# Performance work log

Hardware: AMD Instinct MI355X
Metric: run time of the kernel (lower is better)

Reference implementation:

```python
import jax, jax.numpy as jnp
import numpy as np

B, T = 1, 2048
N_EMBD = 4096
N_HEAD = 32
N_GROUPS = 8
HEAD = 128
Q_PER_KV = N_HEAD // N_GROUPS  # 4
WINDOW = 1024
EPS = 1e-5
ROPE_THETA = 10000.0


def setup_inputs() -> dict:
    key = jax.random.key(0)
    k0, k1, k2 = jax.random.split(key, 3)
    x = jax.random.normal(k0, (B, T, N_EMBD), dtype=jnp.float32)
    # RoPE tables: cos/sin of shape [T, HEAD] (rotary_percentage=1.0)
    inv_freq = 1.0 / (ROPE_THETA ** (jnp.arange(0, HEAD, 2, dtype=jnp.float32) / HEAD))
    ang = jnp.arange(T, dtype=jnp.float32)[:, None] * inv_freq[None, :]  # [T, HEAD//2]
    ang = jnp.concatenate([ang, ang], axis=-1)  # [T, HEAD]
    cos, sin = jnp.cos(ang), jnp.sin(ang)
    qkv_out = (N_HEAD + 2 * N_GROUPS) * HEAD  # 6144
    W_qkv = jax.random.normal(k1, (qkv_out, N_EMBD), dtype=jnp.float32) * 0.02
    W_proj = jax.random.normal(k2, (N_EMBD, N_HEAD * HEAD), dtype=jnp.float32) * 0.02
    norm_q_w = jnp.ones((N_HEAD * HEAD,), dtype=jnp.float32)
    norm_k_w = jnp.ones((N_GROUPS * HEAD,), dtype=jnp.float32)
    return {"x": x, "cos": cos, "sin": sin, "W_qkv": W_qkv,
            "norm_q_w": norm_q_w, "norm_k_w": norm_k_w, "W_proj": W_proj}


def _rmsnorm(x, w):
    # RMSNorm over last dim, matching litgpt RMSNorm (eps inside sqrt)
    var = jnp.mean(x * x, axis=-1, keepdims=True)
    return x * jax.lax.rsqrt(var + EPS) * w


def _apply_rope(x, cos, sin):
    # x: [B, H, T, D]; cos/sin: [T, D] (broadcast over B, H)
    d = x.shape[-1]
    x1, x2 = x[..., : d // 2], x[..., d // 2:]
    rotated = jnp.concatenate([-x2, x1], axis=-1)
    return x * cos + rotated * sin


def reference(x, cos, sin, W_qkv, norm_q_w, norm_k_w, W_proj):
    Bx, Tx, _ = x.shape
    qkv = jnp.einsum('btc,oc->bto', x, W_qkv)  # [B, T, (H+2G)*D]
    q_size = N_HEAD * HEAD
    kv_size = N_GROUPS * HEAD
    q = qkv[..., :q_size]
    k = qkv[..., q_size:q_size + kv_size]
    v = qkv[..., q_size + kv_size:]
    # norm_qk: RMSNorm over the full flattened q / k dims (pre head reshape)
    q = _rmsnorm(q, norm_q_w)
    k = _rmsnorm(k, norm_k_w)
    q = q.reshape(Bx, Tx, N_HEAD, HEAD).transpose(0, 2, 1, 3)     # [B, H, T, D]
    k = k.reshape(Bx, Tx, N_GROUPS, HEAD).transpose(0, 2, 1, 3)   # [B, G, T, D]
    v = v.reshape(Bx, Tx, N_GROUPS, HEAD).transpose(0, 2, 1, 3)   # [B, G, T, D]
    # rope_n_elem == head_size (rotary_percentage = 1.0)
    q = _apply_rope(q, cos, sin)
    k = _apply_rope(k, cos, sin)
    # GQA: expand kv groups to heads (repeat_interleave on head dim)
    k = jnp.repeat(k, Q_PER_KV, axis=1)  # [B, H, T, D]
    v = jnp.repeat(v, Q_PER_KV, axis=1)
    scale = 1.0 / jnp.sqrt(jnp.float32(HEAD))  # attention_scores_scalar is None
    scores = jnp.einsum('bhqd,bhkd->bhqk', q, k) * scale
    # causal + sliding-window mask: allowed iff 0 <= q_idx - kv_idx < WINDOW
    d = jnp.arange(Tx)[:, None] - jnp.arange(Tx)[None, :]
    bias = jnp.where((d >= 0) & (d < WINDOW), 0.0, -jnp.inf).astype(scores.dtype)
    attn = jax.nn.softmax(scores + bias, axis=-1)
    y = jnp.einsum('bhqk,bhkd->bhqd', attn, v)        # [B, H, T, D]
    y = y.transpose(0, 2, 1, 3).reshape(Bx, Tx, N_HEAD * HEAD)
    return jnp.einsum('bth,oh->bto', y, W_proj)       # [B, T, n_embd]
```

## Files before the change

### kernel.cpp

```cpp
#include <hip/hip_runtime.h>
#include <stdint.h>
#include <stddef.h>

#define T_SEQ 2048
#define WINDOW_SZ 1024

typedef __attribute__((ext_vector_type(4))) float f32x4;
typedef __attribute__((ext_vector_type(8))) short s16x8;

__device__ inline unsigned short f2bf(float f) {
  union { float f; unsigned u; } v; v.f = f;
  unsigned u = v.u;
  return (unsigned short)((u + 0x7fffu + ((u >> 16) & 1u)) >> 16);
}

__device__ inline void gld_lds16(const unsigned short* g, unsigned short* l) {
  __builtin_amdgcn_global_load_lds((const __attribute__((address_space(1))) void*)g,
                                   (__attribute__((address_space(3))) void*)l, 16, 0, 0);
}

__global__ __launch_bounds__(256) void cvt_bf16(const float* __restrict__ s,
                                                unsigned short* __restrict__ d, int n4) {
  int i = blockIdx.x * 256 + threadIdx.x;
  if (i >= n4) return;
  float4 v = ((const float4*)s)[i];
  ushort4 o;
  o.x = f2bf(v.x); o.y = f2bf(v.y); o.z = f2bf(v.z); o.w = f2bf(v.w);
  ((ushort4*)d)[i] = o;
}

__global__ __launch_bounds__(256) void gemm_bt(const unsigned short* __restrict__ A,
                                               const unsigned short* __restrict__ Bt,
                                               float* __restrict__ C, int M, int N, int K) {
  __shared__ unsigned short As[4096];
  __shared__ unsigned short Bs[4096];
  const int tid  = threadIdx.x;
  const int wave = tid >> 6, lane = tid & 63;
  const int quad = lane >> 4, l16 = lane & 15;
  const int m0 = blockIdx.y << 7, n0 = blockIdx.x << 7;
  const int wr = (wave >> 1) << 6;
  const int wc = (wave & 1) << 6;
  const int srow = tid >> 2;
  const int scol = (tid & 3) << 3;

  f32x4 acc[4][4] = {};

  const unsigned short* pA0 = A  + (size_t)(m0 + srow) * K + scol;
  const unsigned short* pA1 = A  + (size_t)(m0 + 64 + srow) * K + scol;
  const unsigned short* pB0 = Bt + (size_t)(n0 + srow) * K + scol;
  const unsigned short* pB1 = Bt + (size_t)(n0 + 64 + srow) * K + scol;
  unsigned short* lA0 = As + wave * 512;
  unsigned short* lA1 = As + 2048 + wave * 512;
  unsigned short* lB0 = Bs + wave * 512;
  unsigned short* lB1 = Bs + 2048 + wave * 512;

  for (int k0 = 0; k0 < K; k0 += 32) {
    gld_lds16(pA0 + k0, lA0);
    gld_lds16(pA1 + k0, lA1);
    gld_lds16(pB0 + k0, lB0);
    gld_lds16(pB1 + k0, lB1);
    __syncthreads();
    s16x8 af[4], bfr[4];
#pragma unroll
    for (int i = 0; i < 4; i++) {
      af[i]  = *(const s16x8*)&As[(wr + i * 16 + l16) * 32 + quad * 8];
      bfr[i] = *(const s16x8*)&Bs[(wc + i * 16 + l16) * 32 + quad * 8];
    }
#pragma unroll
    for (int mi = 0; mi < 4; mi++)
#pragma unroll
      for (int ni = 0; ni < 4; ni++)
        acc[mi][ni] = __builtin_amdgcn_mfma_f32_16x16x32_bf16(af[mi], bfr[ni], acc[mi][ni], 0, 0, 0);
    __syncthreads();
  }
#pragma unroll
  for (int mi = 0; mi < 4; mi++)
#pragma unroll
    for (int ni = 0; ni < 4; ni++) {
      int row = m0 + wr + mi * 16 + quad * 4;
      int col = n0 + wc + ni * 16 + l16;
#pragma unroll
      for (int r = 0; r < 4; r++)
        C[(size_t)(row + r) * N + col] = acc[mi][ni][r];
    }
}

__global__ __launch_bounds__(256) void normrope(const float* __restrict__ qkv,
                                                const float* __restrict__ cosb,
                                                const float* __restrict__ sinb,
                                                const float* __restrict__ wq,
                                                const float* __restrict__ wk,
                                                unsigned short* __restrict__ qr,
                                                unsigned short* __restrict__ kr,
                                                unsigned short* __restrict__ vt) {
  const int t = blockIdx.x, tid = threadIdx.x;
  const float* row = qkv + (size_t)t * 6144;
  float sq = 0.f, sk = 0.f;
#pragma unroll
  for (int i = 0; i < 4; i++) {
    float4 v = ((const float4*)row)[tid + i * 256];
    sq += v.x * v.x + v.y * v.y + v.z * v.z + v.w * v.w;
  }
  {
    float4 v = ((const float4*)(row + 4096))[tid];
    sk = v.x * v.x + v.y * v.y + v.z * v.z + v.w * v.w;
  }
#pragma unroll
  for (int off = 32; off; off >>= 1) { sq += __shfl_xor(sq, off); sk += __shfl_xor(sk, off); }
  __shared__ float red[8];
  if ((tid & 63) == 0) { red[tid >> 6] = sq; red[4 + (tid >> 6)] = sk; }
  __syncthreads();
  sq = red[0] + red[1] + red[2] + red[3];
  sk = red[4] + red[5] + red[6] + red[7];
  const float rq = rsqrtf(sq * (1.f / 4096.f) + 1e-5f) * (0.08838834764831845f * 1.4426950408889634f);
  const float rk = rsqrtf(sk * (1.f / 1024.f) + 1e-5f);
  for (int i = tid; i < 4096; i += 256) {
    int h = i >> 7, d = i & 127;
    int pd = (d < 64) ? d + 64 : d - 64;
    float val = row[i] * rq * wq[i];
    float pv  = row[(h << 7) + pd] * rq * wq[(h << 7) + pd];
    float rot = (d < 64) ? -pv : pv;
    float o = val * cosb[t * 128 + d] + rot * sinb[t * 128 + d];
    qr[(size_t)h * T_SEQ * 128 + t * 128 + d] = f2bf(o);
  }
  for (int i = tid; i < 1024; i += 256) {
    int g = i >> 7, d = i & 127;
    int pd = (d < 64) ? d + 64 : d - 64;
    float val = row[4096 + i] * rk * wk[i];
    float pv  = row[4096 + (g << 7) + pd] * rk * wk[(g << 7) + pd];
    float rot = (d < 64) ? -pv : pv;
    float o = val * cosb[t * 128 + d] + rot * sinb[t * 128 + d];
    kr[(size_t)g * T_SEQ * 128 + t * 128 + d] = f2bf(o);
  }
  for (int i = tid; i < 1024; i += 256) {
    int g = i >> 7, d = i & 127;
    vt[(size_t)g * 128 * T_SEQ + (size_t)d * T_SEQ + t] = f2bf(row[5120 + i]);
  }
}

__global__ __launch_bounds__(512, 2) void attn(const unsigned short* __restrict__ Q,
                                               const unsigned short* __restrict__ Kb,
                                               const unsigned short* __restrict__ Vt,
                                               unsigned short* __restrict__ Y) {
  __shared__ unsigned short Kbuf[2][64 * 128];
  __shared__ unsigned short Vbuf[2][128 * 64];
  __shared__ unsigned short Pbuf[8][2][16 * 72];
  const int qb = blockIdx.x, g = blockIdx.y;
  const int tid = threadIdx.x, wave = tid >> 6, lane = tid & 63;
  const int quad = lane >> 4, l16 = lane & 15;
  const int h = g * 4 + (wave >> 1);
  const int qbase = qb * 64;
  const int q0 = qbase + (wave & 1) * 32;
  const unsigned short* Qh = Q + (size_t)h * T_SEQ * 128;
  const unsigned short* Kg = Kb + (size_t)g * T_SEQ * 128;
  const unsigned short* Vg = Vt + (size_t)g * 128 * T_SEQ;

  s16x8 aq[2][4];
#pragma unroll
  for (int qt = 0; qt < 2; qt++)
#pragma unroll
    for (int ks = 0; ks < 4; ks++)
      aq[qt][ks] = *(const s16x8*)&Qh[(size_t)(q0 + qt * 16 + l16) * 128 + ks * 32 + quad * 8];

  f32x4 acc[2][8] = {};
  float lrow[2][4] = {};

  int lo = qbase - (WINDOW_SZ - 1);
  if (lo < 0) lo = 0;
  lo &= ~63;

#define STAGE_CHUNK(buf, kkv)                                                        \
  {                                                                                  \
    int kk_ = (kkv);                                                                 \
    _Pragma("unroll")                                                                \
    for (int j = 0; j < 2; j++) {                                                    \
      int rloc = wave * 8 + j * 4 + (lane >> 4);                                     \
      int oct = (lane & 15) ^ (rloc & 15);                                           \
      gld_lds16(Kg + (size_t)(kk_ + rloc) * 128 + oct * 8,                           \
                &Kbuf[buf][(wave * 8 + j * 4) * 128]);                               \
    }                                                                                \
    _Pragma("unroll")                                                                \
    for (int j = 0; j < 2; j++) {                                                    \
      int dloc = wave * 16 + j * 8 + (lane >> 3);                                    \
      int oct = (lane & 7) ^ (dloc & 7);                                             \
      gld_lds16(Vg + (size_t)dloc * T_SEQ + kk_ + oct * 8,                           \
                &Vbuf[buf][(wave * 16 + j * 8) * 64]);                               \
    }                                                                                \
  }

  STAGE_CHUNK(0, lo);
  int ib = 0;
  for (int kk = lo; kk < qbase + 64; kk += 64, ib ^= 1) {
    __syncthreads();
    if (kk + 64 < qbase + 64) STAGE_CHUNK(ib ^ 1, kk + 64);
    if (kk > q0 + 31 || kk + 63 < q0 - (WINDOW_SZ - 1)) continue;
    const unsigned short* kb = Kbuf[ib];
    const unsigned short* vb = Vbuf[ib];
    f32x4 sc[2][4] = {};
#pragma unroll
    for (int ks = 0; ks < 4; ks++) {
#pragma unroll
      for (int ci = 0; ci < 4; ci++) {
        s16x8 bk = *(const s16x8*)&kb[(ci * 16 + l16) * 128 + (((ks * 4 + quad) ^ l16) * 8)];
        sc[0][ci] = __builtin_amdgcn_mfma_f32_16x16x32_bf16(aq[0][ks], bk, sc[0][ci], 0, 0, 0);
        sc[1][ci] = __builtin_amdgcn_mfma_f32_16x16x32_bf16(aq[1][ks], bk, sc[1][ci], 0, 0, 0);
      }
    }
#pragma unroll
    for (int qt = 0; qt < 2; qt++)
#pragma unroll
      for (int ci = 0; ci < 4; ci++) {
        int col = kk + ci * 16 + l16;
#pragma unroll
        for (int r = 0; r < 4; r++) {
          int irow = q0 + qt * 16 + quad * 4 + r;
          unsigned dd = (unsigned)(irow - col);
          float e = (dd < (unsigned)WINDOW_SZ) ? exp2f(sc[qt][ci][r]) : 0.f;
          lrow[qt][r] += e;
          Pbuf[wave][qt][(quad * 4 + r) * 72 + ci * 16 + l16] = f2bf(e);
        }
      }
#pragma unroll
    for (int c = 0; c < 2; c++) {
      s16x8 pa0 = *(const s16x8*)&Pbuf[wave][0][l16 * 72 + c * 32 + quad * 8];
      s16x8 pa1 = *(const s16x8*)&Pbuf[wave][1][l16 * 72 + c * 32 + quad * 8];
#pragma unroll
      for (int n = 0; n < 8; n++) {
        s16x8 bv = *(const s16x8*)&vb[(n * 16 + l16) * 64 + (((c * 4 + quad) ^ (l16 & 7)) * 8)];
        acc[0][n] = __builtin_amdgcn_mfma_f32_16x16x32_bf16(pa0, bv, acc[0][n], 0, 0, 0);
        acc[1][n] = __builtin_amdgcn_mfma_f32_16x16x32_bf16(pa1, bv, acc[1][n], 0, 0, 0);
      }
    }
  }
#undef STAGE_CHUNK
#pragma unroll
  for (int qt = 0; qt < 2; qt++)
#pragma unroll
    for (int r = 0; r < 4; r++) {
#pragma unroll
      for (int off = 8; off; off >>= 1) lrow[qt][r] += __shfl_xor(lrow[qt][r], off);
      lrow[qt][r] = 1.f / lrow[qt][r];
    }
#pragma unroll
  for (int qt = 0; qt < 2; qt++)
#pragma unroll
    for (int n = 0; n < 8; n++)
#pragma unroll
      for (int r = 0; r < 4; r++) {
        int irow = q0 + qt * 16 + quad * 4 + r;
        Y[(size_t)irow * 4096 + h * 128 + n * 16 + l16] = f2bf(acc[qt][n][r] * lrow[qt][r]);
      }
}

extern "C" void kernel_launch(void* const* d_in, const int* in_sizes, int n_in,
                              void* d_out, int out_size, void* d_ws, size_t ws_size,
                              hipStream_t stream) {
  (void)in_sizes; (void)n_in; (void)out_size; (void)ws_size;
  const float* x     = (const float*)d_in[0];
  const float* cosb  = (const float*)d_in[1];
  const float* sinb  = (const float*)d_in[2];
  const float* Wqkv  = (const float*)d_in[3];
  const float* wq    = (const float*)d_in[4];
  const float* wk    = (const float*)d_in[5];
  const float* Wproj = (const float*)d_in[6];
  float* out = (float*)d_out;

  char* ws = (char*)d_ws;
  unsigned short* x_bf     = (unsigned short*)(ws);
  unsigned short* wqkv_bf  = (unsigned short*)(ws + 16777216);
  unsigned short* wproj_bf = (unsigned short*)(ws + 67108864);
  float*          qkv      = (float*)(ws + 100663296);
  unsigned short* qr       = (unsigned short*)(ws + 150994944);
  unsigned short* kr       = (unsigned short*)(ws + 167772160);
  unsigned short* vt       = (unsigned short*)(ws + 171966464);
  unsigned short* y        = (unsigned short*)(ws + 176160768);

  cvt_bf16<<<(2097152 + 255) / 256, 256, 0, stream>>>(x, x_bf, 2097152);
  cvt_bf16<<<(6291456 + 255) / 256, 256, 0, stream>>>(Wqkv, wqkv_bf, 6291456);
  cvt_bf16<<<(4194304 + 255) / 256, 256, 0, stream>>>(Wproj, wproj_bf, 4194304);
  gemm_bt<<<dim3(48, 16), 256, 0, stream>>>(x_bf, wqkv_bf, qkv, 2048, 6144, 4096);
  normrope<<<2048, 256, 0, stream>>>(qkv, cosb, sinb, wq, wk, qr, kr, vt);
  attn<<<dim3(32, 8), 512, 0, stream>>>(qr, kr, vt, y);
  gemm_bt<<<dim3(32, 16), 256, 0, stream>>>(y, wproj_bf, out, 2048, 4096, 4096);
}
```

Before: 563.6 us.

## Double GEMM K-tile with XOR-swizzled LDS and emit bf16 QKV intermediate

The GEMM now loads a 64-wide K slice per iteration, which halves the barrier count and the number of loop trips. It stores tiles in LDS with an XOR chunk swizzle to avoid bank conflicts on the fragment reads. The QKV projection now writes bf16 instead of fp32, halving the intermediate write and the norm/rope kernel's read traffic. In exchange the q/k values are quantized before RMSNorm, which reduces precision slightly, and the GEMM uses twice the LDS per block.

```diff
diff --git a/kernel.cpp b/kernel.cpp
--- a/kernel.cpp
+++ b/kernel.cpp
@@ -1,23 +1,31 @@
 #include <hip/hip_runtime.h>
 #include <stdint.h>
 #include <stddef.h>
+#include <type_traits>
 
 #define T_SEQ 2048
 #define WINDOW_SZ 1024
 
 typedef __attribute__((ext_vector_type(4))) float f32x4;
 typedef __attribute__((ext_vector_type(8))) short s16x8;
+typedef __attribute__((ext_vector_type(4))) short s16x4;
 
 __device__ inline unsigned short f2bf(float f) {
   union { float f; unsigned u; } v; v.f = f;
   unsigned u = v.u;
   return (unsigned short)((u + 0x7fffu + ((u >> 16) & 1u)) >> 16);
 }
+__device__ inline float bf2f(unsigned short u) {
+  union { unsigned u; float f; } v; v.u = ((unsigned)u) << 16; return v.f;
+}
 
 __device__ inline void gld_lds16(const unsigned short* g, unsigned short* l) {
   __builtin_amdgcn_global_load_lds((const __attribute__((address_space(1))) void*)g,
                                    (__attribute__((address_space(3))) void*)l, 16, 0, 0);
 }
+
+__device__ inline void store_out(float* p, float v) { *p = v; }
+__device__ inline void store_out(unsigned short* p, float v) { *p = f2bf(v); }
 
 __global__ __launch_bounds__(256) void cvt_bf16(const float* __restrict__ s,
                                                 unsigned short* __restrict__ d, int n4) {
@@ -29,48 +37,48 @@
   ((ushort4*)d)[i] = o;
 }
 
+template <typename OutT>
 __global__ __launch_bounds__(256) void gemm_bt(const unsigned short* __restrict__ A,
                                                const unsigned short* __restrict__ Bt,
-                                               float* __restrict__ C, int M, int N, int K) {
-  __shared__ unsigned short As[4096];
-  __shared__ unsigned short Bs[4096];
+                                               OutT* __restrict__ C, int M, int N, int K) {
+  __shared__ unsigned short As[128 * 64];
+  __shared__ unsigned short Bs[128 * 64];
   const int tid  = threadIdx.x;
   const int wave = tid >> 6, lane = tid & 63;
   const int quad = lane >> 4, l16 = lane & 15;
   const int m0 = blockIdx.y << 7, n0 = blockIdx.x << 7;
   const int wr = (wave >> 1) << 6;
   const int wc = (wave & 1) << 6;
-  const int srow = tid >> 2;
-  const int scol = (tid & 3) << 3;
+  const int srow = wave * 8 + (lane >> 3);
+  const int gchunk0 = lane & 7;
 
   f32x4 acc[4][4] = {};
 
-  const unsigned short* pA0 = A  + (size_t)(m0 + srow) * K + scol;
-  const unsigned short* pA1 = A  + (size_t)(m0 + 64 + srow) * K + scol;
-  const unsigned short* pB0 = Bt + (size_t)(n0 + srow) * K + scol;
-  const unsigned short* pB1 = Bt + (size_t)(n0 + 64 + srow) * K + scol;
-  unsigned short* lA0 = As + wave * 512;
-  unsigned short* lA1 = As + 2048 + wave * 512;
-  unsigned short* lB0 = Bs + wave * 512;
-  unsigned short* lB1 = Bs + 2048 + wave * 512;
-
-  for (int k0 = 0; k0 < K; k0 += 32) {
-    gld_lds16(pA0 + k0, lA0);
-    gld_lds16(pA1 + k0, lA1);
-    gld_lds16(pB0 + k0, lB0);
-    gld_lds16(pB1 + k0, lB1);
+  for (int k0 = 0; k0 < K; k0 += 64) {
+#pragma unroll
+    for (int j = 0; j < 4; j++) {
+      int r = j * 32 + srow;
+      int gc = gchunk0 ^ (r & 7);
+      gld_lds16(A  + (size_t)(m0 + r) * K + k0 + gc * 8, &As[(j * 32 + wave * 8) * 64]);
+      gld_lds16(Bt + (size_t)(n0 + r) * K + k0 + gc * 8, &Bs[(j * 32 + wave * 8) * 64]);
+    }
     __syncthreads();
-    s16x8 af[4], bfr[4];
-#pragma unroll
-    for (int i = 0; i < 4; i++) {
-      af[i]  = *(const s16x8*)&As[(wr + i * 16 + l16) * 32 + quad * 8];
-      bfr[i] = *(const s16x8*)&Bs[(wc + i * 16 + l16) * 32 + quad * 8];
-    }
-#pragma unroll
-    for (int mi = 0; mi < 4; mi++)
-#pragma unroll
-      for (int ni = 0; ni < 4; ni++)
-        acc[mi][ni] = __builtin_amdgcn_mfma_f32_16x16x32_bf16(af[mi], bfr[ni], acc[mi][ni], 0, 0, 0);
+#pragma unroll
+    for (int s = 0; s < 2; s++) {
+      s16x8 af[4], bfr[4];
+#pragma unroll
+      for (int i = 0; i < 4; i++) {
+        int ra = wr + i * 16 + l16;
+        af[i]  = *(const s16x8*)&As[ra * 64 + (((s * 4 + quad) ^ (ra & 7)) * 8)];
+        int rb = wc + i * 16 + l16;
+        bfr[i] = *(const s16x8*)&Bs[rb * 64 + (((s * 4 + quad) ^ (rb & 7)) * 8)];
+      }
+#pragma unroll
+      for (int mi = 0; mi < 4; mi++)
+#pragma unroll
+        for (int ni = 0; ni < 4; ni++)
+          acc[mi][ni] = __builtin_amdgcn_mfma_f32_16x16x32_bf16(af[mi], bfr[ni], acc[mi][ni], 0, 0, 0);
+    }
     __syncthreads();
   }
 #pragma unroll
@@ -81,11 +89,11 @@
       int col = n0 + wc + ni * 16 + l16;
 #pragma unroll
       for (int r = 0; r < 4; r++)
-        C[(size_t)(row + r) * N + col] = acc[mi][ni][r];
-    }
-}
-
-__global__ __launch_bounds__(256) void normrope(const float* __restrict__ qkv,
+        store_out(&C[(size_t)(row + r) * N + col], acc[mi][ni][r]);
+    }
+}
+
+__global__ __launch_bounds__(256) void normrope(const unsigned short* __restrict__ qkv,
                                                 const float* __restrict__ cosb,
                                                 const float* __restrict__ sinb,
                                                 const float* __restrict__ wq,
@@ -94,16 +102,24 @@
                                                 unsigned short* __restrict__ kr,
                                                 unsigned short* __restrict__ vt) {
   const int t = blockIdx.x, tid = threadIdx.x;
-  const float* row = qkv + (size_t)t * 6144;
+  const unsigned short* row = qkv + (size_t)t * 6144;
   float sq = 0.f, sk = 0.f;
-#pragma unroll
-  for (int i = 0; i < 4; i++) {
-    float4 v = ((const float4*)row)[tid + i * 256];
-    sq += v.x * v.x + v.y * v.y + v.z * v.z + v.w * v.w;
-  }
   {
-    float4 v = ((const float4*)(row + 4096))[tid];
-    sk = v.x * v.x + v.y * v.y + v.z * v.z + v.w * v.w;
+    s16x8 a = *(const s16x8*)&row[tid * 16];
+    s16x8 b = *(const s16x8*)&row[tid * 16 + 8];
+#pragma unroll
+    for (int j = 0; j < 8; j++) {
+      float fa = bf2f((unsigned short)a[j]), fb = bf2f((unsigned short)b[j]);
+      sq += fa * fa + fb * fb;
+    }
+  }
+  {
+    s16x4 a = *(const s16x4*)&row[4096 + tid * 4];
+#pragma unroll
+    for (int j = 0; j < 4; j++) {
+      float fa = bf2f((unsigned short)a[j]);
+      sk += fa * fa;
+    }
   }
 #pragma unroll
   for (int off = 32; off; off >>= 1) { sq += __shfl_xor(sq, off); sk += __shfl_xor(sk, off); }
@@ -117,8 +133,8 @@
   for (int i = tid; i < 4096; i += 256) {
     int h = i >> 7, d = i & 127;
     int pd = (d < 64) ? d + 64 : d - 64;
-    float val = row[i] * rq * wq[i];
-    float pv  = row[(h << 7) + pd] * rq * wq[(h << 7) + pd];
+    float val = bf2f(row[i]) * rq * wq[i];
+    float pv  = bf2f(row[(h << 7) + pd]) * rq * wq[(h << 7) + pd];
     float rot = (d < 64) ? -pv : pv;
     float o = val * cosb[t * 128 + d] + rot * sinb[t * 128 + d];
     qr[(size_t)h * T_SEQ * 128 + t * 128 + d] = f2bf(o);
@@ -126,15 +142,15 @@
   for (int i = tid; i < 1024; i += 256) {
     int g = i >> 7, d = i & 127;
     int pd = (d < 64) ? d + 64 : d - 64;
-    float val = row[4096 + i] * rk * wk[i];
-    float pv  = row[4096 + (g << 7) + pd] * rk * wk[(g << 7) + pd];
+    float val = bf2f(row[4096 + i]) * rk * wk[i];
+    float pv  = bf2f(row[4096 + (g << 7) + pd]) * rk * wk[(g << 7) + pd];
     float rot = (d < 64) ? -pv : pv;
     float o = val * cosb[t * 128 + d] + rot * sinb[t * 128 + d];
     kr[(size_t)g * T_SEQ * 128 + t * 128 + d] = f2bf(o);
   }
   for (int i = tid; i < 1024; i += 256) {
     int g = i >> 7, d = i & 127;
-    vt[(size_t)g * 128 * T_SEQ + (size_t)d * T_SEQ + t] = f2bf(row[5120 + i]);
+    vt[(size_t)g * 128 * T_SEQ + (size_t)d * T_SEQ + t] = row[5120 + i];
   }
 }
 
@@ -269,7 +285,7 @@
   unsigned short* x_bf     = (unsigned short*)(ws);
   unsigned short* wqkv_bf  = (unsigned short*)(ws + 16777216);
   unsigned short* wproj_bf = (unsigned short*)(ws + 67108864);
-  float*          qkv      = (float*)(ws + 100663296);
+  unsigned short* qkv      = (unsigned short*)(ws + 100663296);
   unsigned short* qr       = (unsigned short*)(ws + 150994944);
   unsigned short* kr       = (unsigned short*)(ws + 167772160);
   unsigned short* vt       = (unsigned short*)(ws + 171966464);
@@ -278,8 +294,8 @@
   cvt_bf16<<<(2097152 + 255) / 256, 256, 0, stream>>>(x, x_bf, 2097152);
   cvt_bf16<<<(6291456 + 255) / 256, 256, 0, stream>>>(Wqkv, wqkv_bf, 6291456);
   cvt_bf16<<<(4194304 + 255) / 256, 256, 0, stream>>>(Wproj, wproj_bf, 4194304);
-  gemm_bt<<<dim3(48, 16), 256, 0, stream>>>(x_bf, wqkv_bf, qkv, 2048, 6144, 4096);
+  gemm_bt<unsigned short><<<dim3(48, 16), 256, 0, stream>>>(x_bf, wqkv_bf, qkv, 2048, 6144, 4096);
   normrope<<<2048, 256, 0, stream>>>(qkv, cosb, sinb, wq, wk, qr, kr, vt);
   attn<<<dim3(32, 8), 512, 0, stream>>>(qr, kr, vt, y);
-  gemm_bt<<<dim3(32, 16), 256, 0, stream>>>(y, wproj_bf, out, 2048, 4096, 4096);
-}
+  gemm_bt<float><<<dim3(32, 16), 256, 0, stream>>>(y, wproj_bf, out, 2048, 4096, 4096);
+}
```

Measured after the change: 519.8 us. 7.8% less time.
